# Optimization experiments

Hardware: AMD Instinct MI355X
Metric: run time of the kernel (lower is better)

## Reference

```python
import jax, jax.numpy as jnp
import numpy as np

ORDER = 4          # signature truncation depth
SCALAR_TERM = True # leading 1 term, as in signatory.signature(..., scalar_term=True)
BATCH, STREAM, CHAN = 2048, 128, 5  # channel = path_dim + 1 (time + 4-dim path)


def _exp_levels(dx, m):
    """Tensor exponential of a single increment dx: levels dx^{(x)k}/k!, k=1..m.
    dx: (B, d). Returns list of (B, d**k) arrays."""
    levels = [dx]
    for k in range(2, m + 1):
        prev = levels[-1]  # (B, d**(k-1))
        levels.append((prev[:, :, None] * dx[:, None, :]).reshape(dx.shape[0], -1) / k)
    return levels


def _chen(S, E):
    """Chen's identity: (S tensor-multiply E) truncated to depth m.
    S, E: tuples/lists of (B, d**k) level arrays (level k at list index k-1)."""
    m = len(E)
    B = E[0].shape[0]
    out = []
    for k in range(m):  # output level k+1
        term = S[k] + E[k]
        for i in range(k):  # S level (i+1) tensor E level (k-i)
            a, b = S[i], E[k - 1 - i]
            term = term + (a[:, :, None] * b[:, None, :]).reshape(B, -1)
        out.append(term)
    return tuple(out)


def _signature(path, m, scalar_term):
    """Truncated path signature, flattened levels 1..m (optionally with leading 1).
    path: (B, T, d) -> (B, [1+] d + d^2 + ... + d^m)."""
    B, T, d = path.shape
    dx = jnp.moveaxis(path[:, 1:] - path[:, :-1], 1, 0)  # (T-1, B, d)
    init = tuple(jnp.zeros((B, d ** k), path.dtype) for k in range(1, m + 1))

    def step(S, inc):
        return _chen(S, _exp_levels(inc, m)), None

    S, _ = jax.lax.scan(step, init, dx)
    sig = jnp.concatenate(S, axis=1)
    if scalar_term:
        sig = jnp.concatenate([jnp.ones((B, 1), path.dtype), sig], axis=1)
    return sig


def setup_inputs() -> dict:
    key = jax.random.key(0)
    kx, ky = jax.random.split(key)
    x = jax.random.normal(kx, (BATCH, STREAM, CHAN), dtype=jnp.float32)
    y = jax.random.normal(ky, (BATCH, STREAM, CHAN), dtype=jnp.float32)
    sigma = jnp.ones((CHAN - 1,), dtype=jnp.float32)  # adversarial scaling params
    return {"x": x, "y": y, "sigma": sigma}


def reference(x, y, sigma):
    # adversarial scaling applied to x's non-time channels only (as in forward())
    mu = jnp.concatenate([x[..., :1], x[..., 1:] * sigma], axis=-1)
    nu = y
    # signatures computed once each and shared across kxx, kxy, kyy (same math)
    sx = _signature(mu, ORDER, SCALAR_TERM)  # (B, P)
    sy = _signature(nu, ORDER, SCALAR_TERM)  # (B, P)
    kxx = jnp.einsum('ip,jp->ij', sx, sx)
    kxy = jnp.einsum('ip,jp->ij', sx, sy)
    kyy = jnp.einsum('ip,jp->ij', sy, sy)
    return jnp.mean(kxx) - 2.0 * jnp.mean(kxy) + jnp.mean(kyy)
```

## Files before the change

kernel.cpp:

```cpp
#include <hip/hip_runtime.h>

#define BATCH  2048
#define TLEN   128
#define CH     5
#define NSTEP  (TLEN - 1)
#define SIGDIM 780
#define KACC   16
#define WPB    4
#define NBLK   ((2 * BATCH) / WPB)

__global__ __launch_bounds__(256) void sig_kernel(
    const float* __restrict__ x, const float* __restrict__ y,
    const float* __restrict__ sigma, float* __restrict__ acc,
    unsigned int* __restrict__ counter, float* __restrict__ out) {
  const int wave = threadIdx.x >> 6;
  const int lane = threadIdx.x & 63;
  const int b    = blockIdx.x * WPB + wave;
  const bool isX = (b < BATCH);
  const int  p   = isX ? b : b - BATCH;
  const float* src = (isX ? x : y) + (size_t)p * (TLEN * CH);

  __shared__ __align__(16) float dxs[WPB][TLEN * 8];
  __shared__ float blockAcc[SIGDIM];
  __shared__ float red[4];
  __shared__ unsigned int lastFlag;

  for (int i = threadIdx.x; i < SIGDIM; i += 256) blockAcc[i] = 0.f;

  float* dxw = dxs[wave];
  for (int i = lane; i < NSTEP * CH; i += 64) {
    int t = i / CH, c = i - CH * t;
    float v = src[i + CH] - src[i];
    if (isX && c > 0) v *= sigma[c - 1];
    dxw[t * 8 + c] = v;
  }
  if (lane < 8) dxw[NSTEP * 8 + lane] = 0.f;
  __syncthreads();

  const int  ab  = (lane >> 1) < 25 ? (lane >> 1) : 24;
  const int  a_  = ab / 5, b_ = ab - 5 * a_;
  const bool odd = (lane & 1);
  const int  c0i = odd ? 3 : 0, c1i = odd ? 4 : 1;
  const bool act = (lane < 50);

  float s1a = 0.f, s2 = 0.f;
  float s30 = 0.f, s31 = 0.f, s32 = 0.f;
  float s40[5] = {0,0,0,0,0}, s41[5] = {0,0,0,0,0}, s42[5] = {0,0,0,0,0};

  float4 dvn = *(const float4*)dxw;
  float  d4n = dxw[4], dan = dxw[a_], dbn = dxw[b_];
  float  dc0n = dxw[c0i], dc1n = dxw[c1i];

  #pragma unroll 4
  for (int t = 0; t < NSTEP; ++t) {
    const float d0 = dvn.x, d1 = dvn.y, d2 = dvn.z, d3 = dvn.w, d4 = d4n;
    const float da = dan, db = dbn, dc0 = dc0n, dc1 = dc1n, dc2 = d2;
    const float* nx = dxw + (t + 1) * 8;
    dvn = *(const float4*)nx;
    d4n = nx[4]; dan = nx[a_]; dbn = nx[b_]; dc0n = nx[c0i]; dc1n = nx[c1i];

    const float pa = s1a * (1.f / 6.f) + da * (1.f / 24.f);
    const float qa = s1a * 0.5f        + da * (1.f / 6.f);
    const float ra = s1a               + da * 0.5f;
    s1a += da;
    const float p2 = 0.5f * s2 + db * pa;
    const float q2 =        s2 + db * qa;
    s2 += db * ra;
    const float p30 = s30 + dc0 * p2;  s30 += dc0 * q2;
    const float p31 = s31 + dc1 * p2;  s31 += dc1 * q2;
    const float p32 = s32 + dc2 * p2;  s32 += dc2 * q2;
    s40[0] += d0 * p30; s40[1] += d1 * p30; s40[2] += d2 * p30; s40[3] += d3 * p30; s40[4] += d4 * p30;
    s41[0] += d0 * p31; s41[1] += d1 * p31; s41[2] += d2 * p31; s41[3] += d3 * p31; s41[4] += d4 * p31;
    s42[0] += d0 * p32; s42[1] += d1 * p32; s42[2] += d2 * p32; s42[3] += d3 * p32; s42[4] += d4 * p32;
  }

  if (act) {
    const int base3 = 30 + ab * 5;
    if ((lane % 10) == 0) atomicAdd(&blockAcc[lane / 10], s1a);
    if (!odd)             atomicAdd(&blockAcc[5 + ab], s2);
    atomicAdd(&blockAcc[base3 + c0i], s30);
    atomicAdd(&blockAcc[base3 + c1i], s31);
    if (!odd) atomicAdd(&blockAcc[base3 + 2], s32);
    const int b40 = 155 + (ab * 5 + c0i) * 5;
    const int b41 = 155 + (ab * 5 + c1i) * 5;
    const int b42 = 155 + (ab * 5 + 2) * 5;
    #pragma unroll
    for (int d = 0; d < 5; ++d) atomicAdd(&blockAcc[b40 + d], s40[d]);
    #pragma unroll
    for (int d = 0; d < 5; ++d) atomicAdd(&blockAcc[b41 + d], s41[d]);
    if (!odd) {
      #pragma unroll
      for (int d = 0; d < 5; ++d) atomicAdd(&blockAcc[b42 + d], s42[d]);
    }
  }
  __syncthreads();

  const float w = (blockIdx.x < (BATCH / WPB)) ? 1.0f : -1.0f;
  float* ap = acc + (size_t)(blockIdx.x & (KACC - 1)) * SIGDIM;
  for (int i = threadIdx.x; i < SIGDIM; i += 256)
    atomicAdd(ap + i, w * blockAcc[i]);

  __syncthreads();
  if (threadIdx.x == 0) {
    __threadfence();
    unsigned int old = __hip_atomic_fetch_add(counter, 1u, __ATOMIC_ACQ_REL,
                                              __HIP_MEMORY_SCOPE_AGENT);
    lastFlag = (old == NBLK - 1) ? 1u : 0u;
  }
  __syncthreads();
  if (lastFlag) {
    const int tid = threadIdx.x;
    float local = 0.f;
    for (int i = tid; i < SIGDIM; i += 256) {
      float v = 0.f;
      #pragma unroll
      for (int k = 0; k < KACC; ++k)
        v += __hip_atomic_load(&acc[(size_t)k * SIGDIM + i],
                               __ATOMIC_RELAXED, __HIP_MEMORY_SCOPE_AGENT);
      local += v * v;
    }
    #pragma unroll
    for (int off = 32; off > 0; off >>= 1) local += __shfl_down(local, off, 64);
    if ((tid & 63) == 0) red[tid >> 6] = local;
    __syncthreads();
    if (tid == 0)
      out[0] = (red[0] + red[1] + red[2] + red[3]) / (2048.0f * 2048.0f);
  }
}

extern "C" void kernel_launch(void* const* d_in, const int* in_sizes, int n_in,
                              void* d_out, int out_size, void* d_ws, size_t ws_size,
                              hipStream_t stream) {
  const float* x     = (const float*)d_in[0];
  const float* y     = (const float*)d_in[1];
  const float* sigma = (const float*)d_in[2];
  float* out = (float*)d_out;
  float* acc = (float*)d_ws;
  unsigned int* counter = (unsigned int*)((char*)d_ws + (size_t)KACC * SIGDIM * sizeof(float));

  hipMemsetAsync(d_ws, 0, (size_t)KACC * SIGDIM * sizeof(float) + 64, stream);
  sig_kernel<<<dim3(NBLK), dim3(256), 0, stream>>>(x, y, sigma, acc, counter, out);
}
```

Before: 118.8 us.

## Split each path scan into two halves combined via Chen's identity

Each path's 127-step scan is split into two segments of 64 and 63 steps, each run on its own wave. The two partial signatures are combined in shared memory with an explicit Chen product, which halves the serial dependency chain per wave at the cost of twice as many waves. Blocks now cover 2 paths instead of 4, so the grid and the launch bounds change, and the shared-memory atomics into the block accumulator become plain stores. The extra combine step and syncs add overhead, and occupancy of 8 blocks per SM may pressure registers.

```diff
diff --git a/kernel.cpp b/kernel.cpp
--- a/kernel.cpp
+++ b/kernel.cpp
@@ -3,38 +3,41 @@
 #define BATCH  2048
 #define TLEN   128
 #define CH     5
-#define NSTEP  (TLEN - 1)
+#define NSTEP  127
+#define HALF1  64
 #define SIGDIM 780
 #define KACC   16
-#define WPB    4
-#define NBLK   ((2 * BATCH) / WPB)
+#define NBLK   2048
 
-__global__ __launch_bounds__(256) void sig_kernel(
+__global__ __launch_bounds__(256, 8) void sig_kernel(
     const float* __restrict__ x, const float* __restrict__ y,
     const float* __restrict__ sigma, float* __restrict__ acc,
     unsigned int* __restrict__ counter, float* __restrict__ out) {
-  const int wave = threadIdx.x >> 6;
-  const int lane = threadIdx.x & 63;
-  const int b    = blockIdx.x * WPB + wave;
-  const bool isX = (b < BATCH);
-  const int  p   = isX ? b : b - BATCH;
-  const float* src = (isX ? x : y) + (size_t)p * (TLEN * CH);
+  const int tid  = threadIdx.x;
+  const int wave = tid >> 6;
+  const int lane = tid & 63;
+  const bool isX = (blockIdx.x < NBLK / 2);
+  const int pbase = isX ? 2 * blockIdx.x : 2 * (blockIdx.x - NBLK / 2);
+  const int path  = pbase + (wave >> 1);
+  const int seg   = wave & 1;
 
-  __shared__ __align__(16) float dxs[WPB][TLEN * 8];
+  __shared__ __align__(16) float wbuf[4][784];
   __shared__ float blockAcc[SIGDIM];
   __shared__ float red[4];
   __shared__ unsigned int lastFlag;
 
-  for (int i = threadIdx.x; i < SIGDIM; i += 256) blockAcc[i] = 0.f;
-
-  float* dxw = dxs[wave];
-  for (int i = lane; i < NSTEP * CH; i += 64) {
-    int t = i / CH, c = i - CH * t;
-    float v = src[i + CH] - src[i];
-    if (isX && c > 0) v *= sigma[c - 1];
-    dxw[t * 8 + c] = v;
+  float* dxw = wbuf[wave];
+  if (lane < 16) dxw[504 + lane] = 0.f;
+  {
+    const float* src = (isX ? x : y) + (size_t)path * (TLEN * CH) + seg * (HALF1 * CH);
+    const int lim = seg ? (63 * CH) : (64 * CH);
+    for (int i = lane; i < lim; i += 64) {
+      int t = i / CH, c = i - CH * t;
+      float v = src[i + CH] - src[i];
+      if (isX && c > 0) v *= sigma[c - 1];
+      dxw[t * 8 + c] = v;
+    }
   }
-  if (lane < 8) dxw[NSTEP * 8 + lane] = 0.f;
   __syncthreads();
 
   const int  ab  = (lane >> 1) < 25 ? (lane >> 1) : 24;
@@ -47,18 +50,16 @@
   float s30 = 0.f, s31 = 0.f, s32 = 0.f;
   float s40[5] = {0,0,0,0,0}, s41[5] = {0,0,0,0,0}, s42[5] = {0,0,0,0,0};
 
-  float4 dvn = *(const float4*)dxw;
-  float  d4n = dxw[4], dan = dxw[a_], dbn = dxw[b_];
-  float  dc0n = dxw[c0i], dc1n = dxw[c1i];
-
   #pragma unroll 4
-  for (int t = 0; t < NSTEP; ++t) {
-    const float d0 = dvn.x, d1 = dvn.y, d2 = dvn.z, d3 = dvn.w, d4 = d4n;
-    const float da = dan, db = dbn, dc0 = dc0n, dc1 = dc1n, dc2 = d2;
-    const float* nx = dxw + (t + 1) * 8;
-    dvn = *(const float4*)nx;
-    d4n = nx[4]; dan = nx[a_]; dbn = nx[b_]; dc0n = nx[c0i]; dc1n = nx[c1i];
-
+  for (int t = 0; t < HALF1; ++t) {
+    const float* row = dxw + t * 8;
+    const float4 dv = *(const float4*)row;
+    const float d0 = dv.x, d1 = dv.y, d2 = dv.z, d3 = dv.w;
+    const float d4 = row[4];
+    const float da  = a_ == 0 ? d0 : a_ == 1 ? d1 : a_ == 2 ? d2 : a_ == 3 ? d3 : d4;
+    const float db  = b_ == 0 ? d0 : b_ == 1 ? d1 : b_ == 2 ? d2 : b_ == 3 ? d3 : d4;
+    const float dc0 = odd ? d3 : d0;
+    const float dc1 = odd ? d4 : d1;
     const float pa = s1a * (1.f / 6.f) + da * (1.f / 24.f);
     const float qa = s1a * 0.5f        + da * (1.f / 6.f);
     const float ra = s1a               + da * 0.5f;
@@ -68,40 +69,78 @@
     s2 += db * ra;
     const float p30 = s30 + dc0 * p2;  s30 += dc0 * q2;
     const float p31 = s31 + dc1 * p2;  s31 += dc1 * q2;
-    const float p32 = s32 + dc2 * p2;  s32 += dc2 * q2;
+    const float p32 = s32 + d2  * p2;  s32 += d2  * q2;
     s40[0] += d0 * p30; s40[1] += d1 * p30; s40[2] += d2 * p30; s40[3] += d3 * p30; s40[4] += d4 * p30;
     s41[0] += d0 * p31; s41[1] += d1 * p31; s41[2] += d2 * p31; s41[3] += d3 * p31; s41[4] += d4 * p31;
     s42[0] += d0 * p32; s42[1] += d1 * p32; s42[2] += d2 * p32; s42[3] += d3 * p32; s42[4] += d4 * p32;
   }
 
-  if (act) {
-    const int base3 = 30 + ab * 5;
-    if ((lane % 10) == 0) atomicAdd(&blockAcc[lane / 10], s1a);
-    if (!odd)             atomicAdd(&blockAcc[5 + ab], s2);
-    atomicAdd(&blockAcc[base3 + c0i], s30);
-    atomicAdd(&blockAcc[base3 + c1i], s31);
-    if (!odd) atomicAdd(&blockAcc[base3 + 2], s32);
-    const int b40 = 155 + (ab * 5 + c0i) * 5;
-    const int b41 = 155 + (ab * 5 + c1i) * 5;
-    const int b42 = 155 + (ab * 5 + 2) * 5;
-    #pragma unroll
-    for (int d = 0; d < 5; ++d) atomicAdd(&blockAcc[b40 + d], s40[d]);
-    #pragma unroll
-    for (int d = 0; d < 5; ++d) atomicAdd(&blockAcc[b41 + d], s41[d]);
-    if (!odd) {
+  {
+    float* sg = wbuf[wave];
+    if (act) {
+      if ((lane % 10) == 0) sg[lane / 10] = s1a;
+      if (!odd)             sg[5 + ab]    = s2;
+      const int base3 = 30 + ab * 5;
+      sg[base3 + c0i] = s30;
+      sg[base3 + c1i] = s31;
+      if (!odd) sg[base3 + 2] = s32;
+      const int b40 = 155 + (ab * 5 + c0i) * 5;
+      const int b41 = 155 + (ab * 5 + c1i) * 5;
+      const int b42 = 155 + (ab * 5 + 2) * 5;
       #pragma unroll
-      for (int d = 0; d < 5; ++d) atomicAdd(&blockAcc[b42 + d], s42[d]);
+      for (int d = 0; d < 5; ++d) sg[b40 + d] = s40[d];
+      #pragma unroll
+      for (int d = 0; d < 5; ++d) sg[b41 + d] = s41[d];
+      if (!odd) {
+        #pragma unroll
+        for (int d = 0; d < 5; ++d) sg[b42 + d] = s42[d];
+      }
     }
   }
   __syncthreads();
 
-  const float w = (blockIdx.x < (BATCH / WPB)) ? 1.0f : -1.0f;
+  const int half = tid >> 7;
+  const int t2   = tid & 127;
+  const float* L = wbuf[2 * half];
+  const float* R = wbuf[2 * half + 1];
+  float o4[5] = {0,0,0,0,0};
+  float o3 = 0.f, o2 = 0.f, o1 = 0.f;
+  if (t2 < 125) {
+    const int abc = t2, abq = abc / 5, c = abc - 5 * abq;
+    const int a = abq / 5, b = abq - 5 * a;
+    const float l1 = L[a], l2 = L[5 + abq], l3 = L[30 + abc];
+    o3 = l3 + R[30 + abc] + l2 * R[c] + l1 * R[5 + b * 5 + c];
+    #pragma unroll
+    for (int d = 0; d < 5; ++d)
+      o4[d] = L[155 + abc * 5 + d] + R[155 + abc * 5 + d]
+            + l3 * R[d] + l2 * R[5 + c * 5 + d] + l1 * R[30 + (b * 5 + c) * 5 + d];
+    if (abc < 25) o2 = L[5 + abc] + R[5 + abc] + L[abc / 5] * R[abc - 5 * (abc / 5)];
+    if (abc < 5)  o1 = L[abc] + R[abc];
+  }
+  if (half == 0 && t2 < 125) {
+    blockAcc[30 + t2] = o3;
+    #pragma unroll
+    for (int d = 0; d < 5; ++d) blockAcc[155 + t2 * 5 + d] = o4[d];
+    if (t2 < 25) blockAcc[5 + t2] = o2;
+    if (t2 < 5)  blockAcc[t2] = o1;
+  }
+  __syncthreads();
+  if (half == 1 && t2 < 125) {
+    blockAcc[30 + t2] += o3;
+    #pragma unroll
+    for (int d = 0; d < 5; ++d) blockAcc[155 + t2 * 5 + d] += o4[d];
+    if (t2 < 25) blockAcc[5 + t2] += o2;
+    if (t2 < 5)  blockAcc[t2] += o1;
+  }
+  __syncthreads();
+
+  const float w = isX ? 1.0f : -1.0f;
   float* ap = acc + (size_t)(blockIdx.x & (KACC - 1)) * SIGDIM;
-  for (int i = threadIdx.x; i < SIGDIM; i += 256)
+  for (int i = tid; i < SIGDIM; i += 256)
     atomicAdd(ap + i, w * blockAcc[i]);
 
   __syncthreads();
-  if (threadIdx.x == 0) {
+  if (tid == 0) {
     __threadfence();
     unsigned int old = __hip_atomic_fetch_add(counter, 1u, __ATOMIC_ACQ_REL,
                                               __HIP_MEMORY_SCOPE_AGENT);
@@ -109,7 +148,6 @@
   }
   __syncthreads();
   if (lastFlag) {
-    const int tid = threadIdx.x;
     float local = 0.f;
     for (int i = tid; i < SIGDIM; i += 256) {
       float v = 0.f;
```

After: 139.2 us. 1.17x slower.

## Split increments into float4 SoA layout and process four steps per block

Applied to the files above, without the earlier changes.

Stores per-step increments as a packed 4-channel array plus a separate fifth-channel array. The loop now loads four steps at a time with wide vector loads and selects per-lane operands with register selects instead of indexed shared loads. This aims to cut LDS load instructions and per-step address arithmetic in the serial scan. It also adds a launch-bounds occupancy hint, which may push the compiler toward tighter register allocation, and the select chains add some ALU work per step.

```diff
diff --git a/kernel.cpp b/kernel.cpp
--- a/kernel.cpp
+++ b/kernel.cpp
@@ -3,38 +3,43 @@
 #define BATCH  2048
 #define TLEN   128
 #define CH     5
-#define NSTEP  (TLEN - 1)
+#define NSTEP  127
+#define NPAD   132
 #define SIGDIM 780
 #define KACC   16
 #define WPB    4
 #define NBLK   ((2 * BATCH) / WPB)
 
-__global__ __launch_bounds__(256) void sig_kernel(
+__global__ __launch_bounds__(256, 4) void sig_kernel(
     const float* __restrict__ x, const float* __restrict__ y,
     const float* __restrict__ sigma, float* __restrict__ acc,
     unsigned int* __restrict__ counter, float* __restrict__ out) {
-  const int wave = threadIdx.x >> 6;
-  const int lane = threadIdx.x & 63;
+  const int tid  = threadIdx.x;
+  const int wave = tid >> 6;
+  const int lane = tid & 63;
   const int b    = blockIdx.x * WPB + wave;
   const bool isX = (b < BATCH);
   const int  p   = isX ? b : b - BATCH;
   const float* src = (isX ? x : y) + (size_t)p * (TLEN * CH);
 
-  __shared__ __align__(16) float dxs[WPB][TLEN * 8];
+  __shared__ __align__(16) float main4[WPB][NPAD * 4];
+  __shared__ __align__(16) float aux  [WPB][NPAD];
   __shared__ float blockAcc[SIGDIM];
   __shared__ float red[4];
   __shared__ unsigned int lastFlag;
 
-  for (int i = threadIdx.x; i < SIGDIM; i += 256) blockAcc[i] = 0.f;
+  for (int i = tid; i < SIGDIM; i += 256) blockAcc[i] = 0.f;
 
-  float* dxw = dxs[wave];
+  float* mw = main4[wave];
+  float* aw = aux[wave];
+  if (lane < 20) mw[NSTEP * 4 + lane] = 0.f;
+  if (lane < 5)  aw[NSTEP + lane]     = 0.f;
   for (int i = lane; i < NSTEP * CH; i += 64) {
     int t = i / CH, c = i - CH * t;
     float v = src[i + CH] - src[i];
     if (isX && c > 0) v *= sigma[c - 1];
-    dxw[t * 8 + c] = v;
+    if (c < 4) mw[t * 4 + c] = v; else aw[t] = v;
   }
-  if (lane < 8) dxw[NSTEP * 8 + lane] = 0.f;
   __syncthreads();
 
   const int  ab  = (lane >> 1) < 25 ? (lane >> 1) : 24;
@@ -47,18 +52,11 @@
   float s30 = 0.f, s31 = 0.f, s32 = 0.f;
   float s40[5] = {0,0,0,0,0}, s41[5] = {0,0,0,0,0}, s42[5] = {0,0,0,0,0};
 
-  float4 dvn = *(const float4*)dxw;
-  float  d4n = dxw[4], dan = dxw[a_], dbn = dxw[b_];
-  float  dc0n = dxw[c0i], dc1n = dxw[c1i];
-
-  #pragma unroll 4
-  for (int t = 0; t < NSTEP; ++t) {
-    const float d0 = dvn.x, d1 = dvn.y, d2 = dvn.z, d3 = dvn.w, d4 = d4n;
-    const float da = dan, db = dbn, dc0 = dc0n, dc1 = dc1n, dc2 = d2;
-    const float* nx = dxw + (t + 1) * 8;
-    dvn = *(const float4*)nx;
-    d4n = nx[4]; dan = nx[a_]; dbn = nx[b_]; dc0n = nx[c0i]; dc1n = nx[c1i];
-
+  auto STEP = [&](float d0, float d1, float d2, float d3, float d4) {
+    const float da  = a_ == 0 ? d0 : a_ == 1 ? d1 : a_ == 2 ? d2 : a_ == 3 ? d3 : d4;
+    const float db  = b_ == 0 ? d0 : b_ == 1 ? d1 : b_ == 2 ? d2 : b_ == 3 ? d3 : d4;
+    const float dc0 = odd ? d3 : d0;
+    const float dc1 = odd ? d4 : d1;
     const float pa = s1a * (1.f / 6.f) + da * (1.f / 24.f);
     const float qa = s1a * 0.5f        + da * (1.f / 6.f);
     const float ra = s1a               + da * 0.5f;
@@ -68,10 +66,30 @@
     s2 += db * ra;
     const float p30 = s30 + dc0 * p2;  s30 += dc0 * q2;
     const float p31 = s31 + dc1 * p2;  s31 += dc1 * q2;
-    const float p32 = s32 + dc2 * p2;  s32 += dc2 * q2;
+    const float p32 = s32 + d2  * p2;  s32 += d2  * q2;
     s40[0] += d0 * p30; s40[1] += d1 * p30; s40[2] += d2 * p30; s40[3] += d3 * p30; s40[4] += d4 * p30;
     s41[0] += d0 * p31; s41[1] += d1 * p31; s41[2] += d2 * p31; s41[3] += d3 * p31; s41[4] += d4 * p31;
     s42[0] += d0 * p32; s42[1] += d1 * p32; s42[2] += d2 * p32; s42[3] += d3 * p32; s42[4] += d4 * p32;
+  };
+
+  float4 m0 = *(const float4*)(mw + 0);
+  float4 m1 = *(const float4*)(mw + 4);
+  float4 m2 = *(const float4*)(mw + 8);
+  float4 m3 = *(const float4*)(mw + 12);
+  float4 a4 = *(const float4*)(aw + 0);
+  for (int blk = 0; blk < 32; ++blk) {
+    const float4 cm0 = m0, cm1 = m1, cm2 = m2, cm3 = m3, ca = a4;
+    const float* mb = mw + (blk + 1) * 16;
+    const float* ab4 = aw + (blk + 1) * 4;
+    m0 = *(const float4*)(mb + 0);
+    m1 = *(const float4*)(mb + 4);
+    m2 = *(const float4*)(mb + 8);
+    m3 = *(const float4*)(mb + 12);
+    a4 = *(const float4*)(ab4);
+    STEP(cm0.x, cm0.y, cm0.z, cm0.w, ca.x);
+    STEP(cm1.x, cm1.y, cm1.z, cm1.w, ca.y);
+    STEP(cm2.x, cm2.y, cm2.z, cm2.w, ca.z);
+    STEP(cm3.x, cm3.y, cm3.z, cm3.w, ca.w);
   }
 
   if (act) {
@@ -95,13 +113,13 @@
   }
   __syncthreads();
 
-  const float w = (blockIdx.x < (BATCH / WPB)) ? 1.0f : -1.0f;
+  const float w = isX ? 1.0f : -1.0f;
   float* ap = acc + (size_t)(blockIdx.x & (KACC - 1)) * SIGDIM;
-  for (int i = threadIdx.x; i < SIGDIM; i += 256)
+  for (int i = tid; i < SIGDIM; i += 256)
     atomicAdd(ap + i, w * blockAcc[i]);
 
   __syncthreads();
-  if (threadIdx.x == 0) {
+  if (tid == 0) {
     __threadfence();
     unsigned int old = __hip_atomic_fetch_add(counter, 1u, __ATOMIC_ACQ_REL,
                                               __HIP_MEMORY_SCOPE_AGENT);
@@ -109,7 +127,6 @@
   }
   __syncthreads();
   if (lastFlag) {
-    const int tid = threadIdx.x;
     float local = 0.f;
     for (int i = tid; i < SIGDIM; i += 256) {
       float v = 0.f;
```

Result: slower. 138.2 us (+16.4%).
